# Kernel tuning notes

Measured on AMD Instinct MI355X. Metric: run time of the kernel, lower is better.

The kernel has to match this reference:

```python
import jax, jax.numpy as jnp
import numpy as np

NUM_HEADS = 16


def setup_inputs() -> dict:
    key = jax.random.key(0)
    ks = jax.random.split(key, 6)
    B, T, C = 2, 1024, 2048
    H, D = NUM_HEADS, C // NUM_HEADS
    Tc = 1024  # cached tokens
    return {
        "x": jax.random.normal(ks[0], (B, T, C), dtype=jnp.float32),
        "cache_k": jax.random.normal(ks[1], (B, H, Tc, D), dtype=jnp.float32),
        "cache_v": jax.random.normal(ks[2], (B, H, Tc, D), dtype=jnp.float32),
        "W_qkv": jax.random.normal(ks[3], (C, 3 * C), dtype=jnp.float32) * (C ** -0.5),
        "W_proj": jax.random.normal(ks[4], (C, C), dtype=jnp.float32) * (C ** -0.5),
        "b_proj": jnp.zeros((C,), dtype=jnp.float32),
        "seq_start": Tc,
    }


def reference(x, cache_k, cache_v, W_qkv, W_proj, b_proj, seq_start):
    B, T, C = x.shape
    H = NUM_HEADS
    D = C // H
    scale = D ** -0.5

    qkv = (x @ W_qkv).reshape(B, T, 3, H, D)
    # (B, H, T, D)
    q = jnp.transpose(qkv[:, :, 0], (0, 2, 1, 3))
    k = jnp.transpose(qkv[:, :, 1], (0, 2, 1, 3))
    v = jnp.transpose(qkv[:, :, 2], (0, 2, 1, 3))

    # append to KV cache along time axis
    k = jnp.concatenate([cache_k, k], axis=2)
    v = jnp.concatenate([cache_v, v], axis=2)
    k_len = k.shape[2]

    # causal mask on absolute positions: query_pos >= key_pos
    query_pos = seq_start + jnp.arange(T)
    key_pos = jnp.arange(k_len)
    causal = query_pos[:, None] >= key_pos[None, :]  # (T, k_len)

    attn = jnp.einsum("bhqd,bhkd->bhqk", q * scale, k)
    attn = jnp.where(causal[None, None], attn, -jnp.inf)
    attn = jax.nn.softmax(attn, axis=-1)

    out = jnp.einsum("bhqk,bhkd->bhqd", attn, v)
    out = jnp.transpose(out, (0, 2, 1, 3)).reshape(B, T, C)
    out = out @ W_proj + b_proj
    return out, k, v
```

## Files before the change

kernel.cpp:

```cpp
#include <hip/hip_runtime.h>
#include <hip/hip_bf16.h>

typedef __attribute__((ext_vector_type(8))) short bf16x8;
typedef __attribute__((ext_vector_type(4))) float f32x4;
typedef __attribute__((ext_vector_type(16))) float f32x16;

#define DI __device__ __forceinline__

static constexpr int Bb  = 2;
static constexpr int Tt  = 1024;
static constexpr int Cc  = 2048;
static constexpr int Hh  = 16;
static constexpr int Dd  = 128;
static constexpr int TC  = 1024;
static constexpr int CTX = 2048;
static constexpr float QSCALE = 0.08838834764831845f;

DI unsigned short f2bf(float f){
  unsigned u = __builtin_bit_cast(unsigned, f);
  u += 0x7FFFu + ((u >> 16) & 1u);
  return (unsigned short)(u >> 16);
}
DI float bf2f(unsigned short s){
  return __builtin_bit_cast(float, (unsigned)s << 16);
}
DI unsigned pk2(float a, float b){
  return (unsigned)f2bf(a) | ((unsigned)f2bf(b) << 16);
}
DI bf16x8 mk4(unsigned a, unsigned b, unsigned c, unsigned d){
  union{ unsigned u[4]; bf16x8 v; } x;
  x.u[0]=a; x.u[1]=b; x.u[2]=c; x.u[3]=d; return x.v;
}
DI f32x16 mfma32(bf16x8 a, bf16x8 b, f32x16 c){
  return __builtin_amdgcn_mfma_f32_32x32x16_bf16(a, b, c, 0, 0, 0);
}
#define MFMA16(a,b,c) __builtin_amdgcn_mfma_f32_16x16x32_bf16(a,b,c,0,0,0)
DI void gld16(const void* g, void* l){
  __builtin_amdgcn_global_load_lds(
      (const __attribute__((address_space(1))) unsigned int*)g,
      (__attribute__((address_space(3))) unsigned int*)l, 16, 0, 0);
}
DI unsigned ldsoff(const void* p){
  return (unsigned)(size_t)(const __attribute__((address_space(3))) void*)p;
}
template<int OFF>
DI bf16x8 dsr(unsigned addr){
  bf16x8 v;
  if constexpr (OFF == 0)
    asm volatile("ds_read_b128 %0, %1" : "=v"(v) : "v"(addr));
  else
    asm volatile("ds_read_b128 %0, %1 offset:%2" : "=v"(v) : "v"(addr), "i"(OFF));
  return v;
}
#define BARNC   asm volatile("s_barrier")
#define LGKM0   asm volatile("s_waitcnt lgkmcnt(0)")
#define VMCNT4  asm volatile("s_waitcnt vmcnt(4)")
#define VMCNT3  asm volatile("s_waitcnt vmcnt(3)")
#define VMCNT0  asm volatile("s_waitcnt vmcnt(0)")
#define SBAR    __builtin_amdgcn_sched_barrier(0)

DI void transpose_body(const float* in, unsigned short* out,
                       int C, int ostride, int r0, int c0, int mode,
                       unsigned short (*tile)[33]){
  int tx = threadIdx.x & 31, ty = threadIdx.x >> 5;
#pragma unroll
  for(int i=0;i<4;i++){
    int r = r0 + ty + i*8;
    tile[ty + i*8][tx] = f2bf(in[(size_t)r * C + c0 + tx]);
  }
  __syncthreads();
#pragma unroll
  for(int i=0;i<4;i++){
    int c = c0 + ty + i*8;
    int k = r0 + tx;
    int kp;
    if(mode == 0)
      kp = (k & ~24) | ((((k>>3)&3) ^ ((c>>1)&3)) << 3);
    else
      kp = (k & ~56) | ((((k>>3)&7) ^ (c&7)) << 3);
    out[(size_t)c * ostride + kp] = tile[tx][ty + i*8];
  }
}

__global__ __launch_bounds__(256) void fused_pre_k(
    const float* __restrict__ W_qkv, unsigned short* __restrict__ WqkvT,
    const float4* __restrict__ x4, unsigned short* __restrict__ xbf,
    const float4* __restrict__ ck, const float4* __restrict__ cv,
    float4* __restrict__ ok, float4* __restrict__ ov,
    unsigned short* __restrict__ Kws,
    const float* __restrict__ W_proj, unsigned short* __restrict__ WprojT,
    unsigned short* __restrict__ Vt){
  __shared__ unsigned short tile[32][33];
  int bid = blockIdx.x;
  if(bid < 12288){
    int bx = bid % 192, by = bid / 192;
    transpose_body(W_qkv, WqkvT, 6144, 2048, by*32, bx*32, 0, tile);
  } else if(bid < 16384){
    int idx = (bid - 12288) * 256 + threadIdx.x;
    int m = idx >> 9;
    int c4 = (idx & 511) * 4;
    float4 v = x4[idx];
    int cp = (c4 & ~24) | ((((c4>>3)&3) ^ ((m>>1)&3)) << 3);
    uint2 p; p.x = pk2(v.x, v.y); p.y = pk2(v.z, v.w);
    *(uint2*)(xbf + (size_t)m * Cc + cp) = p;
  } else if(bid < 20480){
    int idx = (bid - 16384) * 256 + threadIdx.x;
    const int per = TC * Dd / 4;
    int bh = idx / per, r = idx - bh * per;
    int dst = bh * (CTX * Dd / 4) + r;
    float4 kv = ck[idx];
    ok[dst] = kv;
    ov[dst] = cv[idx];
    int key = r >> 5, dq = (r & 31) * 4;
    int dp = (((dq>>3) ^ (key&7)) << 3) | (dq & 7);
    uint2 p; p.x = pk2(kv.x, kv.y); p.y = pk2(kv.z, kv.w);
    *(uint2*)(Kws + ((size_t)bh * CTX + key) * Dd + dp) = p;
  } else if(bid < 24576){
    int b2 = bid - 20480;
    int bx = b2 & 63, by = b2 >> 6;
    transpose_body(W_proj, WprojT, 2048, 2048, by*32, bx*32, 0, tile);
  } else {
    int zz = bid - 24576;
    int bh = zz >> 7, rem = zz & 127;
    int bx = rem & 3, by = rem >> 2;
    transpose_body((const float*)cv + (size_t)bh*131072,
                   Vt + (size_t)bh*262144, 128, CTX, by*32, bx*32, 1, tile);
  }
}

__global__ __launch_bounds__(256, 3) void gemmA_k(
    const unsigned short* __restrict__ A, const unsigned short* __restrict__ BT,
    unsigned short* __restrict__ q_ws, float* __restrict__ out_k,
    float* __restrict__ out_v, unsigned short* __restrict__ Kws,
    unsigned short* __restrict__ Vt){
  __shared__ unsigned short Al[3][128*32];
  __shared__ unsigned short Bl[3][128*32];
  int tid = threadIdx.x, lane = tid & 63, w = tid >> 6;
  int lr = lane & 15, lg = lane >> 4;
  constexpr int NWG = 768;
  int bid = blockIdx.x;
  int swz = (bid & 7) * (NWG/8) + (bid >> 3);
  int m0 = (swz & 15) * 128;
  int n0 = (swz >> 4) * 128;
  int wr = (w >> 1) * 64, wc = (w & 1) * 64;
  int fsw = (lg ^ ((lr >> 1) & 3)) << 3;

  unsigned baseAb = ldsoff(Al) + (unsigned)(((wr + lr)*32 + fsw)*2);
  unsigned baseBb = ldsoff(Bl) + (unsigned)(((wc + lr)*32 + fsw)*2);

  f32x4 acc[4][4];
#pragma unroll
  for(int i=0;i<4;i++)
#pragma unroll
    for(int j=0;j<4;j++) acc[i][j] = (f32x4){0.f,0.f,0.f,0.f};

  auto stage = [&](int buf, int kt){
    int k0 = kt * 32;
#pragma unroll
    for(int li=0; li<2; li++){
      int rb = w*32 + li*16;
      gld16(A  + (size_t)(m0 + rb + (lane>>2))*Cc + k0 + (lane&3)*8, &Al[buf][rb*32]);
      gld16(BT + (size_t)(n0 + rb + (lane>>2))*Cc + k0 + (lane&3)*8, &Bl[buf][rb*32]);
    }
  };

  stage(0, 0); stage(1, 1);
  int bc = 0;
#pragma unroll 1
  for(int s = 0; s < 64; s++){
    SBAR;
    VMCNT4;
    BARNC;
    SBAR;
    int bn2 = bc + 2; if(bn2 >= 3) bn2 -= 3;
    stage(bn2, (s+2)&63);
    SBAR;
    unsigned aA = baseAb + (unsigned)bc*8192u;
    unsigned aB = baseBb + (unsigned)bc*8192u;
    bf16x8 af[4], bfr[4];
    af[0]  = dsr<0>(aA);    af[1]  = dsr<1024>(aA);
    af[2]  = dsr<2048>(aA); af[3]  = dsr<3072>(aA);
    bfr[0] = dsr<0>(aB);    bfr[1] = dsr<1024>(aB);
    bfr[2] = dsr<2048>(aB); bfr[3] = dsr<3072>(aB);
    LGKM0;
    SBAR;
    __builtin_amdgcn_s_setprio(1);
#pragma unroll
    for(int mi=0;mi<4;mi++)
#pragma unroll
      for(int ni=0;ni<4;ni++)
        acc[mi][ni] = MFMA16(af[mi], bfr[ni], acc[mi][ni]);
    __builtin_amdgcn_s_setprio(0);
    SBAR;
    bc += 1; if(bc >= 3) bc = 0;
  }
  VMCNT0;

#pragma unroll
  for(int mi=0;mi<4;mi++){
#pragma unroll
    for(int ni=0;ni<4;ni++){
      int n = n0 + wc + ni*16 + lr;
      int seg = n >> 11;
      int h = (n >> 7) & 15, d = n & 127;
#pragma unroll
      for(int r=0;r<4;r++){
        int mrow = m0 + wr + mi*16 + lg*4 + r;
        float v = acc[mi][ni][r];
        int b = mrow >> 10, t = mrow & 1023;
        if(seg == 0){
          q_ws[((size_t)(b*Hh + h)*Tt + t)*Dd + d] = f2bf(v * QSCALE);
        } else if(seg == 1){
          int key = TC + t;
          size_t base = (size_t)(b*Hh + h)*CTX + key;
          out_k[base*Dd + d] = v;
          int dp = (((d>>3) ^ (key&7)) << 3) | (d & 7);
          Kws[base*Dd + dp] = f2bf(v);
        } else {
          int key = TC + t;
          out_v[((size_t)(b*Hh + h)*CTX + key)*Dd + d] = v;
          int kp = (key & ~56) | ((((key>>3)&7) ^ (d&7)) << 3);
          Vt[(size_t)(b*Hh + h)*(Dd*CTX) + (size_t)d*CTX + kp] = f2bf(v);
        }
      }
    }
  }
}

__global__ __launch_bounds__(256, 4) void gemmp_k(
    const unsigned short* __restrict__ A, const unsigned short* __restrict__ BT,
    const float* __restrict__ bias, float* __restrict__ outp){
  __shared__ unsigned short Al[3][64*32];
  __shared__ unsigned short Bl[3][128*32];
  int tid = threadIdx.x, lane = tid & 63, w = tid >> 6;
  int lr = lane & 15, lg = lane >> 4;
  int bid = blockIdx.x;
  int swz = (bid & 7) * 64 + (bid >> 3);
  int m0 = (swz & 31) * 64;
  int n0 = (swz >> 5) * 128;
  int wm2 = (w >> 1) * 32, wn2 = (w & 1) * 64;
  int fsw = (lg ^ ((lr >> 1) & 3)) << 3;

  unsigned baseAb = ldsoff(Al) + (unsigned)(((wm2 + lr)*32 + fsw)*2);
  unsigned baseBb = ldsoff(Bl) + (unsigned)(((wn2 + lr)*32 + fsw)*2);

  f32x4 acc[2][4];
#pragma unroll
  for(int i=0;i<2;i++)
#pragma unroll
    for(int j=0;j<4;j++) acc[i][j] = (f32x4){0.f,0.f,0.f,0.f};

  auto stage = [&](int buf, int kt){
    int k0 = kt * 32;
    gld16(A + (size_t)(m0 + w*16 + (lane>>2))*Cc + k0 + (lane&3)*8,
          &Al[buf][w*16*32]);
#pragma unroll
    for(int li=0; li<2; li++){
      int rb = w*32 + li*16;
      gld16(BT + (size_t)(n0 + rb + (lane>>2))*Cc + k0 + (lane&3)*8, &Bl[buf][rb*32]);
    }
  };

  stage(0, 0); stage(1, 1);
  int bc = 0;
#pragma unroll 1
  for(int s = 0; s < 64; s++){
    SBAR;
    VMCNT3;
    BARNC;
    SBAR;
    int bn2 = bc + 2; if(bn2 >= 3) bn2 -= 3;
    stage(bn2, (s+2)&63);
    SBAR;
    unsigned aA = baseAb + (unsigned)bc*4096u;
    unsigned aB = baseBb + (unsigned)bc*8192u;
    bf16x8 af[2], bfr[4];
    af[0]  = dsr<0>(aA);    af[1]  = dsr<1024>(aA);
    bfr[0] = dsr<0>(aB);    bfr[1] = dsr<1024>(aB);
    bfr[2] = dsr<2048>(aB); bfr[3] = dsr<3072>(aB);
    LGKM0;
    SBAR;
    __builtin_amdgcn_s_setprio(1);
#pragma unroll
    for(int mi=0;mi<2;mi++)
#pragma unroll
      for(int ni=0;ni<4;ni++)
        acc[mi][ni] = MFMA16(af[mi], bfr[ni], acc[mi][ni]);
    __builtin_amdgcn_s_setprio(0);
    SBAR;
    bc += 1; if(bc >= 3) bc = 0;
  }
  VMCNT0;

#pragma unroll
  for(int mi=0;mi<2;mi++){
#pragma unroll
    for(int ni=0;ni<4;ni++){
      int n = n0 + wn2 + ni*16 + lr;
#pragma unroll
      for(int r=0;r<4;r++){
        int mrow = m0 + wm2 + mi*16 + lg*4 + r;
        outp[(size_t)mrow * Cc + n] = acc[mi][ni][r] + bias[n];
      }
    }
  }
}

__global__ __launch_bounds__(256, 2) void attn_k(
    const unsigned short* __restrict__ q_ws,
    const unsigned short* __restrict__ Kws,
    const unsigned short* __restrict__ Vt,
    float* __restrict__ O0, unsigned short* __restrict__ O1b,
    float* __restrict__ ml){
  __shared__ unsigned short Kl[2][64*128];
  __shared__ unsigned short Vl[2][128*64];
  int tid = threadIdx.x, lane = tid & 63, w = tid >> 6;
  int l31 = lane & 31, hi = lane >> 5, r7 = l31 & 7;
  int qt = blockIdx.x, split = blockIdx.y, bh = blockIdx.z;
  int q0b = qt * 128, qw0 = q0b + w * 32;
  const unsigned short* Kb = Kws + (size_t)bh * CTX * Dd;
  const unsigned short* Vb = Vt  + (size_t)bh * Dd * CTX;

  const unsigned short* qp = q_ws + ((size_t)bh * Tt + qw0 + l31) * Dd + hi * 8;
  bf16x8 qf[8];
#pragma unroll
  for(int ks=0;ks<8;ks++) qf[ks] = *(const bf16x8*)(qp + ks*16);

  f32x16 o[4];
#pragma unroll
  for(int dt=0;dt<4;dt++)
#pragma unroll
    for(int r=0;r<16;r++) o[dt][r] = 0.f;
  float m = -3e38f, l = 0.f;

  int nts = ((TC + q0b + 128) >> 6) >> 1;

  auto stageK = [&](int buf, int j0){
#pragma unroll
    for(int li=0; li<4; li++){
      gld16(Kb + (size_t)(j0 + w*16 + li*4 + (lane>>4))*Dd + (lane&15)*8,
            &Kl[buf][(w*16 + li*4)*128]);
    }
  };
  auto stageV = [&](int buf, int j0){
#pragma unroll
    for(int li=0; li<4; li++){
      gld16(Vb + (size_t)(w*32 + li*8 + (lane>>3))*CTX + j0 + (lane&7)*8,
            &Vl[buf][(w*32 + li*8)*64]);
    }
  };

  stageK(0, split*64); stageV(0, split*64);
  __syncthreads();
  int buf = 0;
#pragma unroll 1
  for(int t = 0; t < nts; t++){
    int j0 = (2*t + split) * 64;
    if(t + 1 < nts){ stageK(buf^1, j0 + 128); stageV(buf^1, j0 + 128); }

    if(j0 <= TC + qw0 + 31){
      f32x16 s0, s1;
#pragma unroll
      for(int r=0;r<16;r++){ s0[r] = 0.f; s1[r] = 0.f; }
#pragma unroll
      for(int ks=0; ks<8; ks++){
        int ub = ((ks*2 + hi) ^ r7) << 3;
        bf16x8 kf0 = *(const bf16x8*)&Kl[buf][l31*128 + ub];
        bf16x8 kf1 = *(const bf16x8*)&Kl[buf][(32+l31)*128 + ub];
        s0 = mfma32(kf0, qf[ks], s0);
        s1 = mfma32(kf1, qf[ks], s1);
      }
      int qabs = TC + qw0 + l31;
      if(j0 + 63 > TC + qw0){
#pragma unroll
        for(int r=0;r<16;r++){
          int kk = (r&3) + 8*(r>>2) + 4*hi;
          if(j0 + kk > qabs)      s0[r] = -1e30f;
          if(j0 + 32 + kk > qabs) s1[r] = -1e30f;
        }
      }
      float tm = fmaxf(s0[0], s1[0]);
#pragma unroll
      for(int r=1;r<16;r++) tm = fmaxf(tm, fmaxf(s0[r], s1[r]));
      tm = fmaxf(tm, __shfl_xor(tm, 32, 64));
      if(!__all(tm - m <= 8.f)){
        float mn = fmaxf(m, tm);
        float alpha = __expf(m - mn);
        m = mn;
        l *= alpha;
        float ar[16];
#pragma unroll
        for(int r=0;r<16;r++){
          int kk = (r&3) + 8*(r>>2) + 4*hi;
          ar[r] = __shfl(alpha, kk, 64);
        }
#pragma unroll
        for(int dt=0;dt<4;dt++)
#pragma unroll
          for(int r=0;r<16;r++) o[dt][r] *= ar[r];
      }
#pragma unroll
      for(int r=0;r<16;r++){ s0[r] = __expf(s0[r] - m); s1[r] = __expf(s1[r] - m); }
      float ts = 0.f;
#pragma unroll
      for(int r=0;r<16;r++) ts += s0[r] + s1[r];
      ts += __shfl_xor(ts, 32, 64);
      l += ts;
#pragma unroll
      for(int ks16=0; ks16<4; ks16++){
        f32x16 p = (ks16 & 2) ? s1 : s0;
        int fb = (ks16 & 1) * 8;
        unsigned e0 = pk2(p[fb+0], p[fb+1]);
        unsigned e1 = pk2(p[fb+2], p[fb+3]);
        unsigned e2 = pk2(p[fb+4], p[fb+5]);
        unsigned e3 = pk2(p[fb+6], p[fb+7]);
        unsigned x0 = __shfl_xor(e0, 32, 64);
        unsigned x1 = __shfl_xor(e1, 32, 64);
        unsigned x2 = __shfl_xor(e2, 32, 64);
        unsigned x3 = __shfl_xor(e3, 32, 64);
        bf16x8 pa = mk4(hi ? x2 : e0, hi ? x3 : e1, hi ? e2 : x0, hi ? e3 : x1);
        int ub = ((ks16*2 + hi) ^ r7) << 3;
#pragma unroll
        for(int dt=0; dt<4; dt++){
          bf16x8 vf = *(const bf16x8*)&Vl[buf][(dt*32 + l31)*64 + ub];
          o[dt] = mfma32(pa, vf, o[dt]);
        }
      }
    }
    __syncthreads();
    buf ^= 1;
  }

  if(split == 0){
#pragma unroll
    for(int dt=0; dt<4; dt++)
#pragma unroll
      for(int r=0; r<16; r++){
        int q = qw0 + (r&3) + 8*(r>>2) + 4*hi;
        O0[((size_t)bh*Tt + q)*Dd + dt*32 + l31] = o[dt][r];
      }
  } else {
#pragma unroll
    for(int dt=0; dt<4; dt++)
#pragma unroll
      for(int r=0; r<16; r++){
        int q = qw0 + (r&3) + 8*(r>>2) + 4*hi;
        O1b[((size_t)bh*Tt + q)*Dd + dt*32 + l31] = f2bf(o[dt][r]);
      }
  }
  if(lane < 32){
    float* mlp = ml + (((size_t)split*32 + bh)*Tt + qw0 + l31)*2;
    mlp[0] = m; mlp[1] = l;
  }
}

__global__ __launch_bounds__(256) void combine_k(
    const float* __restrict__ O0, const unsigned short* __restrict__ O1b,
    const float* __restrict__ ml, unsigned short* __restrict__ attn_ws){
  int tid = threadIdx.x;
  int d = tid & 127, rl = tid >> 7;
  int row = blockIdx.x * 2 + rl;
  int bh = row >> 10, t = row & 1023;
  const float* p0 = ml + ((size_t)bh * Tt + t) * 2;
  const float* p1 = ml + (((size_t)32 + bh) * Tt + t) * 2;
  float m0 = p0[0], l0 = p0[1], m1 = p1[0], l1 = p1[1];
  float M = fmaxf(m0, m1);
  float e0 = __expf(m0 - M), e1 = __expf(m1 - M);
  float inv = 1.f / (l0*e0 + l1*e1);
  size_t off = (size_t)row * Dd + d;
  float v = (O0[off]*e0 + bf2f(O1b[off])*e1) * inv;
  int b = bh >> 4, h = bh & 15;
  int mrow = b * Tt + t;
  int c = h * Dd + d;
  int cp = (c & ~24) | ((((c>>3)&3) ^ ((mrow>>1)&3)) << 3);
  attn_ws[(size_t)mrow * Cc + cp] = f2bf(v);
}

extern "C" void kernel_launch(void* const* d_in, const int* in_sizes, int n_in,
                              void* d_out, int out_size, void* d_ws, size_t ws_size,
                              hipStream_t stream){
  const float* x       = (const float*)d_in[0];
  const float* cache_k = (const float*)d_in[1];
  const float* cache_v = (const float*)d_in[2];
  const float* W_qkv   = (const float*)d_in[3];
  const float* W_proj  = (const float*)d_in[4];
  const float* b_proj  = (const float*)d_in[5];

  float* out   = (float*)d_out;
  float* out_k = out   + (size_t)Bb*Tt*Cc;
  float* out_v = out_k + (size_t)Bb*Hh*CTX*Dd;
  unsigned short* Vt = (unsigned short*)out;

  if(ws_size < (size_t)67108864) return;
  char* ws = (char*)d_ws;
  unsigned short* WqkvT  = (unsigned short*)(ws);
  float*          O0     = (float*)(ws);
  float*          ml     = (float*)(ws + 16777216);
  unsigned short* WprojT = (unsigned short*)(ws + 25165824);
  unsigned short* Kws    = (unsigned short*)(ws + 33554432);
  unsigned short* attn_ws= (unsigned short*)(ws + 33554432);
  unsigned short* q_ws   = (unsigned short*)(ws + 50331648);
  unsigned short* x_bf   = (unsigned short*)(ws + 58720256);
  unsigned short* O1b    = (unsigned short*)(ws + 58720256);

  fused_pre_k<<<dim3(28672), 256, 0, stream>>>(
      W_qkv, WqkvT, (const float4*)x, x_bf,
      (const float4*)cache_k, (const float4*)cache_v,
      (float4*)out_k, (float4*)out_v, Kws, W_proj, WprojT, Vt);
  gemmA_k<<<dim3(768), 256, 0, stream>>>(x_bf, WqkvT, q_ws, out_k, out_v, Kws, Vt);
  attn_k<<<dim3(8,2,32), 256, 0, stream>>>(q_ws, Kws, Vt, O0, O1b, ml);
  combine_k<<<dim3(16384), 256, 0, stream>>>(O0, O1b, ml, attn_ws);
  gemmp_k<<<dim3(512), 256, 0, stream>>>(attn_ws, WprojT, b_proj, out);
}
```

Measured before the change: 211.2 us.

## Unify QKV and projection GEMMs into templated 64x128 tile kernel with double buffering

Both GEMMs now share one template kernel using 64x128 tiles, a two-stage LDS double buffer with an extra barrier per K step, and launch bounds raised to 6 blocks per CU. The QKV GEMM goes from 768 blocks of 128x128 tiles to 1536 blocks of 64x128, aiming for better occupancy and smaller LDS use. The cost is lower data reuse per tile, since more A and B traffic is loaded per FLOP. The pipeline is also shallower (two buffers instead of three, with a second barrier per step), which may expose more load latency.

Measured after the change: 246.3 us. 1.17x slower.

```diff
diff --git a/kernel.cpp b/kernel.cpp
--- a/kernel.cpp
+++ b/kernel.cpp
@@ -54,7 +54,6 @@
 }
 #define BARNC   asm volatile("s_barrier")
 #define LGKM0   asm volatile("s_waitcnt lgkmcnt(0)")
-#define VMCNT4  asm volatile("s_waitcnt vmcnt(4)")
 #define VMCNT3  asm volatile("s_waitcnt vmcnt(3)")
 #define VMCNT0  asm volatile("s_waitcnt vmcnt(0)")
 #define SBAR    __builtin_amdgcn_sched_barrier(0)
@@ -128,121 +127,26 @@
   }
 }
 
-__global__ __launch_bounds__(256, 3) void gemmA_k(
+template<int EPI, int NWG>
+__global__ __launch_bounds__(256, 6) void gemm_t(
     const unsigned short* __restrict__ A, const unsigned short* __restrict__ BT,
     unsigned short* __restrict__ q_ws, float* __restrict__ out_k,
     float* __restrict__ out_v, unsigned short* __restrict__ Kws,
-    unsigned short* __restrict__ Vt){
-  __shared__ unsigned short Al[3][128*32];
-  __shared__ unsigned short Bl[3][128*32];
-  int tid = threadIdx.x, lane = tid & 63, w = tid >> 6;
-  int lr = lane & 15, lg = lane >> 4;
-  constexpr int NWG = 768;
-  int bid = blockIdx.x;
-  int swz = (bid & 7) * (NWG/8) + (bid >> 3);
-  int m0 = (swz & 15) * 128;
-  int n0 = (swz >> 4) * 128;
-  int wr = (w >> 1) * 64, wc = (w & 1) * 64;
-  int fsw = (lg ^ ((lr >> 1) & 3)) << 3;
-
-  unsigned baseAb = ldsoff(Al) + (unsigned)(((wr + lr)*32 + fsw)*2);
-  unsigned baseBb = ldsoff(Bl) + (unsigned)(((wc + lr)*32 + fsw)*2);
-
-  f32x4 acc[4][4];
-#pragma unroll
-  for(int i=0;i<4;i++)
-#pragma unroll
-    for(int j=0;j<4;j++) acc[i][j] = (f32x4){0.f,0.f,0.f,0.f};
-
-  auto stage = [&](int buf, int kt){
-    int k0 = kt * 32;
-#pragma unroll
-    for(int li=0; li<2; li++){
-      int rb = w*32 + li*16;
-      gld16(A  + (size_t)(m0 + rb + (lane>>2))*Cc + k0 + (lane&3)*8, &Al[buf][rb*32]);
-      gld16(BT + (size_t)(n0 + rb + (lane>>2))*Cc + k0 + (lane&3)*8, &Bl[buf][rb*32]);
-    }
-  };
-
-  stage(0, 0); stage(1, 1);
-  int bc = 0;
-#pragma unroll 1
-  for(int s = 0; s < 64; s++){
-    SBAR;
-    VMCNT4;
-    BARNC;
-    SBAR;
-    int bn2 = bc + 2; if(bn2 >= 3) bn2 -= 3;
-    stage(bn2, (s+2)&63);
-    SBAR;
-    unsigned aA = baseAb + (unsigned)bc*8192u;
-    unsigned aB = baseBb + (unsigned)bc*8192u;
-    bf16x8 af[4], bfr[4];
-    af[0]  = dsr<0>(aA);    af[1]  = dsr<1024>(aA);
-    af[2]  = dsr<2048>(aA); af[3]  = dsr<3072>(aA);
-    bfr[0] = dsr<0>(aB);    bfr[1] = dsr<1024>(aB);
-    bfr[2] = dsr<2048>(aB); bfr[3] = dsr<3072>(aB);
-    LGKM0;
-    SBAR;
-    __builtin_amdgcn_s_setprio(1);
-#pragma unroll
-    for(int mi=0;mi<4;mi++)
-#pragma unroll
-      for(int ni=0;ni<4;ni++)
-        acc[mi][ni] = MFMA16(af[mi], bfr[ni], acc[mi][ni]);
-    __builtin_amdgcn_s_setprio(0);
-    SBAR;
-    bc += 1; if(bc >= 3) bc = 0;
-  }
-  VMCNT0;
-
-#pragma unroll
-  for(int mi=0;mi<4;mi++){
-#pragma unroll
-    for(int ni=0;ni<4;ni++){
-      int n = n0 + wc + ni*16 + lr;
-      int seg = n >> 11;
-      int h = (n >> 7) & 15, d = n & 127;
-#pragma unroll
-      for(int r=0;r<4;r++){
-        int mrow = m0 + wr + mi*16 + lg*4 + r;
-        float v = acc[mi][ni][r];
-        int b = mrow >> 10, t = mrow & 1023;
-        if(seg == 0){
-          q_ws[((size_t)(b*Hh + h)*Tt + t)*Dd + d] = f2bf(v * QSCALE);
-        } else if(seg == 1){
-          int key = TC + t;
-          size_t base = (size_t)(b*Hh + h)*CTX + key;
-          out_k[base*Dd + d] = v;
-          int dp = (((d>>3) ^ (key&7)) << 3) | (d & 7);
-          Kws[base*Dd + dp] = f2bf(v);
-        } else {
-          int key = TC + t;
-          out_v[((size_t)(b*Hh + h)*CTX + key)*Dd + d] = v;
-          int kp = (key & ~56) | ((((key>>3)&7) ^ (d&7)) << 3);
-          Vt[(size_t)(b*Hh + h)*(Dd*CTX) + (size_t)d*CTX + kp] = f2bf(v);
-        }
-      }
-    }
-  }
-}
-
-__global__ __launch_bounds__(256, 4) void gemmp_k(
-    const unsigned short* __restrict__ A, const unsigned short* __restrict__ BT,
+    unsigned short* __restrict__ Vt,
     const float* __restrict__ bias, float* __restrict__ outp){
-  __shared__ unsigned short Al[3][64*32];
-  __shared__ unsigned short Bl[3][128*32];
+  __shared__ unsigned short Al[2][64*32];
+  __shared__ unsigned short Bl[2][128*32];
   int tid = threadIdx.x, lane = tid & 63, w = tid >> 6;
   int lr = lane & 15, lg = lane >> 4;
   int bid = blockIdx.x;
-  int swz = (bid & 7) * 64 + (bid >> 3);
+  int swz = (bid & 7) * (NWG/8) + (bid >> 3);
   int m0 = (swz & 31) * 64;
   int n0 = (swz >> 5) * 128;
-  int wm2 = (w >> 1) * 32, wn2 = (w & 1) * 64;
+  int wr = (w >> 1) * 32, wc = (w & 1) * 64;
   int fsw = (lg ^ ((lr >> 1) & 3)) << 3;
 
-  unsigned baseAb = ldsoff(Al) + (unsigned)(((wm2 + lr)*32 + fsw)*2);
-  unsigned baseBb = ldsoff(Bl) + (unsigned)(((wn2 + lr)*32 + fsw)*2);
+  unsigned baseAb = ldsoff(Al) + (unsigned)(((wr + lr)*32 + fsw)*2);
+  unsigned baseBb = ldsoff(Bl) + (unsigned)(((wc + lr)*32 + fsw)*2);
 
   f32x4 acc[2][4];
 #pragma unroll
@@ -250,8 +154,7 @@
 #pragma unroll
     for(int j=0;j<4;j++) acc[i][j] = (f32x4){0.f,0.f,0.f,0.f};
 
-  auto stage = [&](int buf, int kt){
-    int k0 = kt * 32;
+  auto stage = [&](int buf, int k0){
     gld16(A + (size_t)(m0 + w*16 + (lane>>2))*Cc + k0 + (lane&3)*8,
           &Al[buf][w*16*32]);
 #pragma unroll
@@ -260,20 +163,22 @@
       gld16(BT + (size_t)(n0 + rb + (lane>>2))*Cc + k0 + (lane&3)*8, &Bl[buf][rb*32]);
     }
   };
-
-  stage(0, 0); stage(1, 1);
-  int bc = 0;
+  stage(0, 0);
+  int buf = 0;
 #pragma unroll 1
-  for(int s = 0; s < 64; s++){
+  for(int k0 = 0; k0 < Cc; k0 += 32){
     SBAR;
-    VMCNT3;
+    if(k0 + 32 < Cc){
+      stage(buf^1, k0 + 32);
+      SBAR;
+      VMCNT3;
+    } else {
+      SBAR;
+      VMCNT0;
+    }
     BARNC;
-    SBAR;
-    int bn2 = bc + 2; if(bn2 >= 3) bn2 -= 3;
-    stage(bn2, (s+2)&63);
-    SBAR;
-    unsigned aA = baseAb + (unsigned)bc*4096u;
-    unsigned aB = baseBb + (unsigned)bc*8192u;
+    unsigned aA = baseAb + (unsigned)buf*4096u;
+    unsigned aB = baseBb + (unsigned)buf*8192u;
     bf16x8 af[2], bfr[4];
     af[0]  = dsr<0>(aA);    af[1]  = dsr<1024>(aA);
     bfr[0] = dsr<0>(aB);    bfr[1] = dsr<1024>(aB);
@@ -288,19 +193,40 @@
         acc[mi][ni] = MFMA16(af[mi], bfr[ni], acc[mi][ni]);
     __builtin_amdgcn_s_setprio(0);
     SBAR;
-    bc += 1; if(bc >= 3) bc = 0;
-  }
-  VMCNT0;
+    BARNC;
+    buf ^= 1;
+  }
 
 #pragma unroll
   for(int mi=0;mi<2;mi++){
 #pragma unroll
     for(int ni=0;ni<4;ni++){
-      int n = n0 + wn2 + ni*16 + lr;
+      int n = n0 + wc + ni*16 + lr;
 #pragma unroll
       for(int r=0;r<4;r++){
-        int mrow = m0 + wm2 + mi*16 + lg*4 + r;
-        outp[(size_t)mrow * Cc + n] = acc[mi][ni][r] + bias[n];
+        int mrow = m0 + wr + mi*16 + lg*4 + r;
+        float v = acc[mi][ni][r];
+        if constexpr (EPI == 0){
+          int seg = n >> 11;
+          int h = (n >> 7) & 15, d = n & 127;
+          int b = mrow >> 10, t = mrow & 1023;
+          if(seg == 0){
+            q_ws[((size_t)(b*Hh + h)*Tt + t)*Dd + d] = f2bf(v * QSCALE);
+          } else if(seg == 1){
+            int key = TC + t;
+            size_t base = (size_t)(b*Hh + h)*CTX + key;
+            out_k[base*Dd + d] = v;
+            int dp = (((d>>3) ^ (key&7)) << 3) | (d & 7);
+            Kws[base*Dd + dp] = f2bf(v);
+          } else {
+            int key = TC + t;
+            out_v[((size_t)(b*Hh + h)*CTX + key)*Dd + d] = v;
+            int kp = (key & ~56) | ((((key>>3)&7) ^ (d&7)) << 3);
+            Vt[(size_t)(b*Hh + h)*(Dd*CTX) + (size_t)d*CTX + kp] = f2bf(v);
+          }
+        } else {
+          outp[(size_t)mrow * Cc + n] = v + bias[n];
+        }
       }
     }
   }
@@ -507,8 +433,10 @@
       W_qkv, WqkvT, (const float4*)x, x_bf,
       (const float4*)cache_k, (const float4*)cache_v,
       (float4*)out_k, (float4*)out_v, Kws, W_proj, WprojT, Vt);
-  gemmA_k<<<dim3(768), 256, 0, stream>>>(x_bf, WqkvT, q_ws, out_k, out_v, Kws, Vt);
+  gemm_t<0,1536><<<dim3(1536), 256, 0, stream>>>(x_bf, WqkvT, q_ws, out_k, out_v,
+                                                 Kws, Vt, nullptr, nullptr);
   attn_k<<<dim3(8,2,32), 256, 0, stream>>>(q_ws, Kws, Vt, O0, O1b, ml);
   combine_k<<<dim3(16384), 256, 0, stream>>>(O0, O1b, ml, attn_ws);
-  gemmp_k<<<dim3(512), 256, 0, stream>>>(attn_ws, WprojT, b_proj, out);
-}
+  gemm_t<1,512><<<dim3(512), 256, 0, stream>>>(attn_ws, WprojT, nullptr, nullptr,
+                                               nullptr, nullptr, nullptr, b_proj, out);
+}
```
